# Kernel optimization log

Hardware: AMD Instinct MI355X
Metric: run time of the kernel (lower is better)

Reference implementation:

```python
import jax, jax.numpy as jnp
import numpy as np

N, E, F = 32768, 524288, 16          # nodes, edges, num_filters
S_IN, V_IN = 64, 32                  # input irreps: 64x0e + 32x1o  (dim 64 + 96 = 160)
NRBF = 32                            # radial basis size of f_ij
LN2 = float(np.log(2.0))

def ssp(x):
    # shifted softplus, the standard SchNet activation
    return jax.nn.softplus(x) - LN2

def setup_inputs() -> dict:
    key = jax.random.key(0)
    ks = jax.random.split(key, 16)
    x = jax.random.normal(ks[0], (N, S_IN + 3 * V_IN), jnp.float32)
    idx_i = jax.random.randint(ks[1], (E,), 0, N)
    idx_j = jax.random.randint(ks[2], (E,), 0, N)
    f_ij = jax.random.normal(ks[3], (E, NRBF), jnp.float32)
    rcut_ij = jax.random.uniform(ks[4], (E,), jnp.float32)
    Yr_ij = jax.random.normal(ks[5], (E, 4), jnp.float32)  # 1x0e + 1x1o
    # equivariant Linear 1: (64x0e+32x1o) -> num_filters*(1x0e+1x1o) = 16x0e+16x1o
    W1_0e = jax.random.normal(ks[6], (S_IN, F), jnp.float32)
    W1_1o = jax.random.normal(ks[7], (V_IN, F), jnp.float32)
    # filter MLP: NRBF -> F -> num_irreps(6*F)
    mW1 = jax.random.normal(ks[8], (NRBF, F), jnp.float32) / np.sqrt(NRBF)
    mb1 = jnp.zeros((F,), jnp.float32)
    mW2 = jax.random.normal(ks[9], (F, 6 * F), jnp.float32) / np.sqrt(F)
    mb2 = jnp.zeros((6 * F,), jnp.float32)
    # equivariant Linear 2: (2Fx0e+2Fx1o+Fx1e+Fx2e) -> input irreps (1e/2e paths drop)
    W2_0e = jax.random.normal(ks[10], (2 * F, S_IN), jnp.float32)
    W2_1o = jax.random.normal(ks[11], (2 * F, V_IN), jnp.float32)
    # equivariant Linear 3: input irreps -> input irreps
    W3_0e = jax.random.normal(ks[12], (S_IN, S_IN), jnp.float32)
    W3_1o = jax.random.normal(ks[13], (V_IN, V_IN), jnp.float32)
    return dict(x=x, f_ij=f_ij, rcut_ij=rcut_ij, Yr_ij=Yr_ij,
                W1_0e=W1_0e, W1_1o=W1_1o, mW1=mW1, mb1=mb1, mW2=mW2, mb2=mb2,
                W2_0e=W2_0e, W2_1o=W2_1o, W3_0e=W3_0e, W3_1o=W3_1o,
                idx_i=idx_i, idx_j=idx_j)

def reference(x, f_ij, rcut_ij, Yr_ij, W1_0e, W1_1o, mW1, mb1, mW2, mb2,
              W2_0e, W2_1o, W3_0e, W3_1o, idx_i, idx_j):
    n = x.shape[0]
    s = x[:, :S_IN]                                  # [N, 64]  0e channels
    v = x[:, S_IN:].reshape(n, V_IN, 3)              # [N, 32, 3] 1o channels
    # Linear 1 (per-irrep channel mixing, e3nn fan-in normalization)
    s1 = (s @ W1_0e) / np.sqrt(S_IN)                 # [N, F]
    v1 = jnp.einsum('ncd,cf->nfd', v, W1_1o) / np.sqrt(V_IN)  # [N, F, 3]
    # gather neighbor features (x_j = x[idx_j], mul_to_axis -> per-filter irreps)
    sj = s1[idx_j]                                   # [E, F]
    vj = v1[idx_j]                                   # [E, F, 3]
    y0 = Yr_ij[:, 0]                                 # [E]
    y1 = Yr_ij[:, 1:4]                               # [E, 3]
    # tensor product (0e+1o) x (0e+1o) -> 2x0e + 2x1o + 1x1e + 1x2e, per filter
    o0a = sj * y0[:, None]                                            # 0e: 0e x 0e
    o0b = jnp.einsum('efd,ed->ef', vj, y1) / np.sqrt(3.0)             # 0e: 1o.1o
    o1a = sj[:, :, None] * y1[:, None, :]                             # 1o: 0e x 1o
    o1b = vj * y0[:, None, None]                                      # 1o: 1o x 0e
    o1e = jnp.cross(vj, y1[:, None, :]) / np.sqrt(2.0)                # 1e: 1o ^ 1o
    ux, uy, uz = vj[..., 0], vj[..., 1], vj[..., 2]
    wx, wy, wz = y1[:, None, 0], y1[:, None, 1], y1[:, None, 2]
    o2 = jnp.stack([(ux * wy + uy * wx) / np.sqrt(2.0),
                    (uy * wz + uz * wy) / np.sqrt(2.0),
                    (2.0 * uz * wz - ux * wx - uy * wy) / np.sqrt(6.0),
                    (ux * wz + uz * wx) / np.sqrt(2.0),
                    (ux * wx - uy * wy) / np.sqrt(2.0)], axis=-1)      # 2e [E, F, 5]
    # filter MLP on radial features, gated by cutoff; one scalar per irrep
    W = ssp(f_ij @ mW1 + mb1) @ mW2 + mb2            # [E, 6F]
    W = W * rcut_ij[:, None]
    w0a, w0b, w1a, w1b, w1e, w2 = (W[:, k * F:(k + 1) * F] for k in range(6))
    seg = lambda z: jax.ops.segment_sum(z, idx_i, num_segments=N)
    # modulate + scatter-sum into center atoms
    n0a = seg(o0a * w0a); n0b = seg(o0b * w0b)                          # [N, F]
    n1a = seg(o1a * w1a[:, :, None]); n1b = seg(o1b * w1b[:, :, None])  # [N, F, 3]
    n1e = seg(o1e * w1e[:, :, None])                                    # [N, F, 3] (dropped by Linear 2)
    n2 = seg(o2 * w2[:, :, None])                                       # [N, F, 5] (dropped by Linear 2)
    n0 = jnp.concatenate([n0a, n0b], axis=-1)        # [N, 2F] 0e
    n1 = jnp.concatenate([n1a, n1b], axis=1)         # [N, 2F, 3] 1o
    del n1e, n2  # no matching output irrep in input_irreps -> e3nn Linear drops them
    # Linear 2 back to input irreps
    s2 = (n0 @ W2_0e) / np.sqrt(2 * F)               # [N, 64]
    v2 = jnp.einsum('nfd,fc->ncd', n1, W2_1o) / np.sqrt(2 * F)  # [N, 32, 3]
    # scalar activation on l=0 only
    s2 = ssp(s2)
    # Linear 3
    s3 = (s2 @ W3_0e) / np.sqrt(S_IN)
    v3 = jnp.einsum('ncd,ce->ned', v2, W3_1o) / np.sqrt(V_IN)
    return jnp.concatenate([s3, v3.reshape(n, -1)], axis=-1)  # [N, 160]
```

## Files before the change

### kernel.cpp

```cpp
#include <hip/hip_runtime.h>
#include <math.h>

#define NN 32768
#define NE 524288
#define RSTR 32
#define SREC_STR 36

__device__ __forceinline__ float sspf(float x) {
    const float INVLN2 = 1.4426950408889634f;
    const float LN2    = 0.69314718055994530942f;
    float t = __builtin_amdgcn_exp2f(-fabsf(x) * INVLN2);
    return fmaxf(x, 0.0f) + LN2 * __builtin_amdgcn_logf(1.0f + t) - LN2;
}

__global__ __launch_bounds__(256) void hist_kernel(
    const int* __restrict__ idx_i, int* __restrict__ counts, int* __restrict__ rank)
{
    int e = blockIdx.x * 256 + threadIdx.x;
    rank[e] = atomicAdd(&counts[idx_i[e]], 1);
}

__global__ __launch_bounds__(1024) void scan_kernel(
    const int* __restrict__ counts, int* __restrict__ start, int* __restrict__ order)
{
    __shared__ int tmp[1024];
    __shared__ int bins[64];
    __shared__ int bcur[64];
    int tid = threadIdx.x;
    int base = tid * 32;
    int cnt[32];
    int local[32];
    int sum = 0;
    const int4* c4 = (const int4*)(counts + base);
#pragma unroll
    for (int q = 0; q < 8; q++) {
        int4 v = c4[q];
        cnt[q*4+0] = v.x; cnt[q*4+1] = v.y; cnt[q*4+2] = v.z; cnt[q*4+3] = v.w;
        local[q*4+0] = sum; sum += v.x;
        local[q*4+1] = sum; sum += v.y;
        local[q*4+2] = sum; sum += v.z;
        local[q*4+3] = sum; sum += v.w;
    }
    tmp[tid] = sum;
    __syncthreads();
    for (int off = 1; off < 1024; off <<= 1) {
        int v = 0;
        if (tid >= off) v = tmp[tid - off];
        __syncthreads();
        if (tid >= off) tmp[tid] += v;
        __syncthreads();
    }
    int excl = tmp[tid] - sum;
#pragma unroll
    for (int k = 0; k < 32; k++) {
        start[base + k] = excl + local[k];
    }
    if (tid == 1023) start[NN] = tmp[1023];

    if (tid < 64) bins[tid] = 0;
    __syncthreads();
#pragma unroll
    for (int k = 0; k < 32; k++) {
        int d = cnt[k] > 63 ? 63 : cnt[k];
        atomicAdd(&bins[63 - d], 1);
    }
    __syncthreads();
    if (tid == 0) {
        int run = 0;
        for (int b = 0; b < 64; b++) { int c = bins[b]; bcur[b] = run; run += c; }
    }
    __syncthreads();
#pragma unroll
    for (int k = 0; k < 32; k++) {
        int d = cnt[k] > 63 ? 63 : cnt[k];
        int pos = atomicAdd(&bcur[63 - d], 1);
        order[pos] = base + k;
    }
}

__global__ __launch_bounds__(256) void pack_kernel(
    const float* __restrict__ f_ij,
    const float* __restrict__ rcut_ij,
    const float* __restrict__ Yr,
    const int*   __restrict__ idx_i,
    const int*   __restrict__ idx_j,
    const float* __restrict__ mW1,
    const float* __restrict__ mb1,
    const int*   __restrict__ start,
    const int*   __restrict__ rank,
    float* __restrict__ epack)
{
    __shared__ float sW1[512];
    __shared__ float sb1[16];
    __shared__ float srec[256 * SREC_STR];
    __shared__ int   sslot[256];
    int t = threadIdx.x;
    for (int k = t; k < 512; k += 256) sW1[k] = mW1[k];
    if (t < 16) sb1[t] = mb1[t];
    __syncthreads();

    int e = blockIdx.x * 256 + t;
    float h[16];
#pragma unroll
    for (int f = 0; f < 16; f++) h[f] = sb1[f];
    const float4* frow = (const float4*)(f_ij + (size_t)e * 32);
#pragma unroll
    for (int rq = 0; rq < 8; rq++) {
        float4 fv = frow[rq];
        int r = rq * 4;
#pragma unroll
        for (int f = 0; f < 16; f++)
            h[f] += fv.x * sW1[(r+0)*16+f] + fv.y * sW1[(r+1)*16+f]
                  + fv.z * sW1[(r+2)*16+f] + fv.w * sW1[(r+3)*16+f];
    }
    float rc = rcut_ij[e];
#pragma unroll
    for (int f = 0; f < 16; f++) h[f] = sspf(h[f]) * rc;

    int i = idx_i[e];
    int j = idx_j[e];
    float4 y = ((const float4*)Yr)[e];
    int slot = start[i] + rank[e];

    float* rp = srec + t * SREC_STR;
    float4* rp4 = (float4*)rp;
#pragma unroll
    for (int q = 0; q < 4; q++) rp4[q] = ((float4*)h)[q];
    rp4[4] = y;
    float4 tail; tail.x = rc; tail.y = __int_as_float(j); tail.z = 0.f; tail.w = 0.f;
    rp4[5] = tail;
    float4 z; z.x = 0.f; z.y = 0.f; z.z = 0.f; z.w = 0.f;
    rp4[6] = z;
    rp4[7] = z;
    sslot[t] = slot;
    __syncthreads();

    int lane = t & 63;
    int wbase = t & 192;
    int qi = lane & 7;
#pragma unroll
    for (int g = 0; g < 8; g++) {
        int r = wbase + g * 8 + (lane >> 3);
        int s = sslot[r];
        float4 v = ((const float4*)(srec + r * SREC_STR))[qi];
        ((float4*)(epack + (size_t)s * RSTR))[qi] = v;
    }
}

__global__ __launch_bounds__(256) void embed_kernel(
    const float* __restrict__ x,
    const float* __restrict__ W1s,
    const float* __restrict__ W1v,
    float* __restrict__ embed)
{
    __shared__ float sWs[1024];
    __shared__ float sWv[512];
    int t = threadIdx.x;
    for (int k = t; k < 1024; k += 256) sWs[k] = W1s[k];
    for (int k = t; k < 512;  k += 256) sWv[k] = W1v[k];
    __syncthreads();

    int n = blockIdx.x * 256 + t;
    const float* xr = x + (size_t)n * 160;

    float s1[16];
#pragma unroll
    for (int f = 0; f < 16; f++) s1[f] = 0.f;
#pragma unroll 1
    for (int cc = 0; cc < 4; cc++) {
        float4 sv[4];
#pragma unroll
        for (int q = 0; q < 4; q++) sv[q] = ((const float4*)xr)[cc*4 + q];
#pragma unroll
        for (int q = 0; q < 4; q++) {
            int c = (cc*4 + q) * 4;
#pragma unroll
            for (int f = 0; f < 16; f++) {
                s1[f] += sv[q].x * sWs[(c+0)*16+f] + sv[q].y * sWs[(c+1)*16+f]
                       + sv[q].z * sWs[(c+2)*16+f] + sv[q].w * sWs[(c+3)*16+f];
            }
        }
    }

    float v1[48];
#pragma unroll
    for (int k = 0; k < 48; k++) v1[k] = 0.f;
#pragma unroll 1
    for (int cc = 0; cc < 4; cc++) {
        float4 vv[6];
#pragma unroll
        for (int q = 0; q < 6; q++) vv[q] = ((const float4*)(xr + 64))[cc*6 + q];
#pragma unroll
        for (int q = 0; q < 6; q++) {
            float vals[4] = {vv[q].x, vv[q].y, vv[q].z, vv[q].w};
#pragma unroll
            for (int u = 0; u < 4; u++) {
                int ml = q * 4 + u;
                int c = cc * 8 + ml / 3;
                int d = ml % 3;
                float val = vals[u];
#pragma unroll
                for (int f = 0; f < 16; f++)
                    v1[f*3+d] += val * sWv[c*16+f];
            }
        }
    }

    float ob[64];
    const float is32 = 0.17677669529663688f;
#pragma unroll
    for (int f = 0; f < 16; f++) {
        ob[f*4+0] = s1[f] * 0.125f;
        ob[f*4+1] = v1[f*3+0] * is32;
        ob[f*4+2] = v1[f*3+1] * is32;
        ob[f*4+3] = v1[f*3+2] * is32;
    }

    float4* eo = (float4*)(embed + (size_t)n * 64);
#pragma unroll
    for (int q = 0; q < 16; q++) eo[q] = ((float4*)ob)[q];
}

__global__ __launch_bounds__(256, 4) void nodeagg_kernel(
    const float* __restrict__ embed,
    const float* __restrict__ epack,
    const int*   __restrict__ start,
    const int*   __restrict__ order,
    const float* __restrict__ mW2,
    const float* __restrict__ mb2,
    float* __restrict__ acc)
{
    int t = threadIdx.x;
    int gid = blockIdx.x * 256 + t;
    int node = order[gid >> 4];
    int f = gid & 15;

    float wga[16], wgb[16], wgc[16], wgd[16];
#pragma unroll
    for (int k = 0; k < 16; k++) {
        wga[k] = mW2[k*96 + f];
        wgb[k] = mW2[k*96 + 16 + f];
        wgc[k] = mW2[k*96 + 32 + f];
        wgd[k] = mW2[k*96 + 48 + f];
    }
    float b0a = mb2[f], b0b = mb2[16+f], b1a = mb2[32+f], b1b = mb2[48+f];

    float aa = 0.f, ab = 0.f;
    float A1a0 = 0.f, A1a1 = 0.f, A1a2 = 0.f;
    float A1b0 = 0.f, A1b1 = 0.f, A1b2 = 0.f;

    int s0 = start[node];
    int s1 = start[node+1];

    for (int q = s0; q < s1; q++) {
        const float4* r4 = (const float4*)(epack + (size_t)q * RSTR);
        float4 h0 = r4[0], h1 = r4[1], h2 = r4[2], h3 = r4[3];
        float4 y  = r4[4], tl = r4[5];
        int j = __float_as_int(tl.y);
        float4 e4 = ((const float4*)(embed + (size_t)j * 64))[f];
        float rc = tl.x;

        float w0a = rc*b0a, w0b = rc*b0b, w1a = rc*b1a, w1b = rc*b1b;
        w0a += h0.x*wga[0]  + h0.y*wga[1]  + h0.z*wga[2]  + h0.w*wga[3]
             + h1.x*wga[4]  + h1.y*wga[5]  + h1.z*wga[6]  + h1.w*wga[7]
             + h2.x*wga[8]  + h2.y*wga[9]  + h2.z*wga[10] + h2.w*wga[11]
             + h3.x*wga[12] + h3.y*wga[13] + h3.z*wga[14] + h3.w*wga[15];
        w0b += h0.x*wgb[0]  + h0.y*wgb[1]  + h0.z*wgb[2]  + h0.w*wgb[3]
             + h1.x*wgb[4]  + h1.y*wgb[5]  + h1.z*wgb[6]  + h1.w*wgb[7]
             + h2.x*wgb[8]  + h2.y*wgb[9]  + h2.z*wgb[10] + h2.w*wgb[11]
             + h3.x*wgb[12] + h3.y*wgb[13] + h3.z*wgb[14] + h3.w*wgb[15];
        w1a += h0.x*wgc[0]  + h0.y*wgc[1]  + h0.z*wgc[2]  + h0.w*wgc[3]
             + h1.x*wgc[4]  + h1.y*wgc[5]  + h1.z*wgc[6]  + h1.w*wgc[7]
             + h2.x*wgc[8]  + h2.y*wgc[9]  + h2.z*wgc[10] + h2.w*wgc[11]
             + h3.x*wgc[12] + h3.y*wgc[13] + h3.z*wgc[14] + h3.w*wgc[15];
        w1b += h0.x*wgd[0]  + h0.y*wgd[1]  + h0.z*wgd[2]  + h0.w*wgd[3]
             + h1.x*wgd[4]  + h1.y*wgd[5]  + h1.z*wgd[6]  + h1.w*wgd[7]
             + h2.x*wgd[8]  + h2.y*wgd[9]  + h2.z*wgd[10] + h2.w*wgd[11]
             + h3.x*wgd[12] + h3.y*wgd[13] + h3.z*wgd[14] + h3.w*wgd[15];

        float sj = e4.x, vx = e4.y, vy = e4.z, vz = e4.w;
        aa += sj * y.x * w0a;
        ab += (vx*y.y + vy*y.z + vz*y.w) * w0b;
        float sw = sj * w1a;
        A1a0 += sw * y.y;
        A1a1 += sw * y.z;
        A1a2 += sw * y.w;
        float yw = y.x * w1b;
        A1b0 += vx * yw;
        A1b1 += vy * yw;
        A1b2 += vz * yw;
    }

    const float is3 = 0.5773502691896258f;
    float* o = acc + (size_t)node * 128;
    o[f]       = aa;
    o[16 + f]  = ab * is3;
    o[32 + f]  = A1a0;
    o[48 + f]  = A1a1;
    o[64 + f]  = A1a2;
    o[80 + f]  = A1b0;
    o[96 + f]  = A1b1;
    o[112 + f] = A1b2;
}


__device__ __forceinline__ void v2_seg32(const float* a, int d, int cb,
    const float* __restrict__ W2v, float* V2, int ln)
{
    cb = __builtin_amdgcn_readfirstlane(cb);
    const float is32 = 0.17677669529663688f;
    float na[16], nb[16];
    const float4* pa = (const float4*)(a + 32 + 16*d);
    const float4* pb = (const float4*)(a + 80 + 16*d);
#pragma unroll
    for (int q = 0; q < 4; q++) { ((float4*)na)[q] = pa[q]; ((float4*)nb)[q] = pb[q]; }
    float tacc[32];
#pragma unroll
    for (int c = 0; c < 32; c++) tacc[c] = 0.f;
#pragma unroll
    for (int f = 0; f < 16; f++) {
        float fa = na[f], fb = nb[f];
#pragma unroll
        for (int c = 0; c < 32; c++)
            tacc[c] += fa * W2v[f*32 + cb + c] + fb * W2v[(16+f)*32 + cb + c];
    }
    float* row = V2 + (d*64 + ln) * 33 + cb;
#pragma unroll
    for (int c = 0; c < 32; c++) row[c] = tacc[c] * is32;
}

__device__ __forceinline__ void v2_seg16(const float* a, int d, int cb,
    const float* __restrict__ W2v, float* V2, int ln)
{
    cb = __builtin_amdgcn_readfirstlane(cb);
    const float is32 = 0.17677669529663688f;
    float na[16], nb[16];
    const float4* pa = (const float4*)(a + 32 + 16*d);
    const float4* pb = (const float4*)(a + 80 + 16*d);
#pragma unroll
    for (int q = 0; q < 4; q++) { ((float4*)na)[q] = pa[q]; ((float4*)nb)[q] = pb[q]; }
    float tacc[16];
#pragma unroll
    for (int c = 0; c < 16; c++) tacc[c] = 0.f;
#pragma unroll
    for (int f = 0; f < 16; f++) {
        float fa = na[f], fb = nb[f];
#pragma unroll
        for (int c = 0; c < 16; c++)
            tacc[c] += fa * W2v[f*32 + cb + c] + fb * W2v[(16+f)*32 + cb + c];
    }
    float* row = V2 + (d*64 + ln) * 33 + cb;
#pragma unroll
    for (int c = 0; c < 16; c++) row[c] = tacc[c] * is32;
}

__device__ __forceinline__ void v3_seg32(float* o, int d, int cb,
    const float* __restrict__ W3v, const float* V2, int ln)
{
    cb = __builtin_amdgcn_readfirstlane(cb);
    const float is32 = 0.17677669529663688f;
    float tacc[32];
#pragma unroll
    for (int c = 0; c < 32; c++) tacc[c] = 0.f;
    const float* row = V2 + (d*64 + ln) * 33;
#pragma unroll
    for (int k = 0; k < 32; k++) {
        float vk = row[k];
#pragma unroll
        for (int c = 0; c < 32; c++) tacc[c] += vk * W3v[k*32 + cb + c];
    }
#pragma unroll
    for (int c = 0; c < 32; c++) o[64 + (cb+c)*3 + d] = tacc[c] * is32;
}

__device__ __forceinline__ void v3_seg16(float* o, int d, int cb,
    const float* __restrict__ W3v, const float* V2, int ln)
{
    cb = __builtin_amdgcn_readfirstlane(cb);
    const float is32 = 0.17677669529663688f;
    float tacc[16];
#pragma unroll
    for (int c = 0; c < 16; c++) tacc[c] = 0.f;
    const float* row = V2 + (d*64 + ln) * 33;
#pragma unroll
    for (int k = 0; k < 32; k++) {
        float vk = row[k];
#pragma unroll
        for (int c = 0; c < 16; c++) tacc[c] += vk * W3v[k*32 + cb + c];
    }
#pragma unroll
    for (int c = 0; c < 16; c++) o[64 + (cb+c)*3 + d] = tacc[c] * is32;
}

__global__ __launch_bounds__(256) void out_kernel(
    const float* __restrict__ acc,
    const float* __restrict__ W2s,
    const float* __restrict__ W2v,
    const float* __restrict__ W3s,
    const float* __restrict__ W3v,
    float* __restrict__ out)
{
    __shared__ float S2[64*65];
    __shared__ float V2[3*64*33];
    int t = threadIdx.x;
    int w = t >> 6, ln = t & 63;
    int node = blockIdx.x * 64 + ln;
    const float* a = acc + (size_t)node * 128;
    float* o = out + (size_t)node * 160;
    const float is32 = 0.17677669529663688f;

    if (w < 2) {
        int cb = __builtin_amdgcn_readfirstlane(w * 32);
        float n0r[32];
#pragma unroll
        for (int q = 0; q < 8; q++) ((float4*)n0r)[q] = ((const float4*)a)[q];
        float tacc[32];
#pragma unroll
        for (int c = 0; c < 32; c++) tacc[c] = 0.f;
#pragma unroll
        for (int k = 0; k < 32; k++) {
            float nk = n0r[k];
#pragma unroll
            for (int c = 0; c < 32; c++) tacc[c] += nk * W2s[k*64 + cb + c];
        }
        float* row = S2 + ln*65 + cb;
#pragma unroll
        for (int c = 0; c < 32; c++) row[c] = sspf(tacc[c] * is32);
    } else if (w == 2) {
        v2_seg32(a, 0, 0,  W2v, V2, ln);
        v2_seg16(a, 1, 0,  W2v, V2, ln);
    } else {
        v2_seg16(a, 1, 16, W2v, V2, ln);
        v2_seg32(a, 2, 0,  W2v, V2, ln);
    }
    __syncthreads();
    if (w < 2) {
        int cb = __builtin_amdgcn_readfirstlane(w * 32);
        float tacc[32];
#pragma unroll
        for (int c = 0; c < 32; c++) tacc[c] = 0.f;
        const float* row = S2 + ln*65;
#pragma unroll
        for (int k = 0; k < 64; k++) {
            float sk = row[k];
#pragma unroll
            for (int c = 0; c < 32; c++) tacc[c] += sk * W3s[k*64 + cb + c];
        }
#pragma unroll
        for (int q = 0; q < 8; q++) {
            float4 r = {tacc[q*4+0]*0.125f, tacc[q*4+1]*0.125f,
                        tacc[q*4+2]*0.125f, tacc[q*4+3]*0.125f};
            ((float4*)(o + cb))[q] = r;
        }
    } else if (w == 2) {
        v3_seg32(o, 0, 0,  W3v, V2, ln);
        v3_seg16(o, 1, 0,  W3v, V2, ln);
    } else {
        v3_seg16(o, 1, 16, W3v, V2, ln);
        v3_seg32(o, 2, 0,  W3v, V2, ln);
    }
}

extern "C" void kernel_launch(void* const* d_in, const int* in_sizes, int n_in,
                              void* d_out, int out_size, void* d_ws, size_t ws_size,
                              hipStream_t stream) {
    const float* x     = (const float*)d_in[0];
    const float* f_ij  = (const float*)d_in[1];
    const float* rcut  = (const float*)d_in[2];
    const float* Yr    = (const float*)d_in[3];
    const float* W1s   = (const float*)d_in[4];
    const float* W1v   = (const float*)d_in[5];
    const float* mW1   = (const float*)d_in[6];
    const float* mb1   = (const float*)d_in[7];
    const float* mW2   = (const float*)d_in[8];
    const float* mb2   = (const float*)d_in[9];
    const float* W2s   = (const float*)d_in[10];
    const float* W2v   = (const float*)d_in[11];
    const float* W3s   = (const float*)d_in[12];
    const float* W3v   = (const float*)d_in[13];
    const int*   idx_i = (const int*)d_in[14];
    const int*   idx_j = (const int*)d_in[15];
    float* out = (float*)d_out;

    float* fws   = (float*)d_ws;
    float* embed = fws;
    float* acc   = embed + (size_t)NN * 64;
    float* epack = acc   + (size_t)NN * 128;
    int* ibase   = (int*)(epack + (size_t)NE * RSTR);
    int* counts  = ibase;
    int* start   = counts + NN;
    int* rank    = start + NN + 1;
    int* order   = rank + NE;

    hipMemsetAsync(counts, 0, (size_t)NN * sizeof(int), stream);
    hist_kernel<<<NE/256, 256, 0, stream>>>(idx_i, counts, rank);
    scan_kernel<<<1, 1024, 0, stream>>>(counts, start, order);
    pack_kernel<<<NE/256, 256, 0, stream>>>(f_ij, rcut, Yr, idx_i, idx_j,
                                            mW1, mb1, start, rank, epack);
    embed_kernel<<<NN/256, 256, 0, stream>>>(x, W1s, W1v, embed);
    nodeagg_kernel<<<(NN*16)/256, 256, 0, stream>>>(embed, epack, start, order,
                                                    mW2, mb2, acc);
    out_kernel<<<NN/64, 256, 0, stream>>>(acc, W2s, W2v, W3s, W3v, out);
}
```

Baseline: 333.7 us.

## Halve pack staging LDS and split out_kernel work across eight waves

The pack kernel now stages edge records through a 128-row shared buffer in two passes, each followed by a barrier. This halves LDS use per block so more blocks can be resident. The out kernel moves to 512 threads with eight waves, so each wave keeps smaller accumulator arrays (16 or 24 columns instead of 32). That should lower register pressure and raise occupancy, at the cost of extra barriers and more duplicated reads of the acc rows.

```diff
diff --git a/kernel.cpp b/kernel.cpp
--- a/kernel.cpp
+++ b/kernel.cpp
@@ -92,8 +92,8 @@
 {
     __shared__ float sW1[512];
     __shared__ float sb1[16];
-    __shared__ float srec[256 * SREC_STR];
-    __shared__ int   sslot[256];
+    __shared__ float srec[128 * SREC_STR];
+    __shared__ int   sslot[128];
     int t = threadIdx.x;
     for (int k = t; k < 512; k += 256) sW1[k] = mW1[k];
     if (t < 16) sb1[t] = mb1[t];
@@ -122,28 +122,34 @@
     float4 y = ((const float4*)Yr)[e];
     int slot = start[i] + rank[e];
 
-    float* rp = srec + t * SREC_STR;
-    float4* rp4 = (float4*)rp;
-#pragma unroll
-    for (int q = 0; q < 4; q++) rp4[q] = ((float4*)h)[q];
-    rp4[4] = y;
-    float4 tail; tail.x = rc; tail.y = __int_as_float(j); tail.z = 0.f; tail.w = 0.f;
-    rp4[5] = tail;
-    float4 z; z.x = 0.f; z.y = 0.f; z.z = 0.f; z.w = 0.f;
-    rp4[6] = z;
-    rp4[7] = z;
-    sslot[t] = slot;
-    __syncthreads();
-
-    int lane = t & 63;
-    int wbase = t & 192;
-    int qi = lane & 7;
-#pragma unroll
-    for (int g = 0; g < 8; g++) {
-        int r = wbase + g * 8 + (lane >> 3);
-        int s = sslot[r];
-        float4 v = ((const float4*)(srec + r * SREC_STR))[qi];
-        ((float4*)(epack + (size_t)s * RSTR))[qi] = v;
+#pragma unroll 1
+    for (int p = 0; p < 2; p++) {
+        if ((t >> 7) == p) {
+            int r = t & 127;
+            float* rp = srec + r * SREC_STR;
+            float4* rp4 = (float4*)rp;
+#pragma unroll
+            for (int q = 0; q < 4; q++) rp4[q] = ((float4*)h)[q];
+            rp4[4] = y;
+            float4 tail; tail.x = rc; tail.y = __int_as_float(j);
+            tail.z = 0.f; tail.w = 0.f;
+            rp4[5] = tail;
+            float4 z; z.x = 0.f; z.y = 0.f; z.z = 0.f; z.w = 0.f;
+            rp4[6] = z;
+            rp4[7] = z;
+            sslot[r] = slot;
+        }
+        __syncthreads();
+#pragma unroll
+        for (int g = 0; g < 4; g++) {
+            int idx = g * 256 + t;
+            int r = idx >> 3;
+            int qi = idx & 7;
+            int s = sslot[r];
+            float4 v = ((const float4*)(srec + r * SREC_STR))[qi];
+            ((float4*)(epack + (size_t)s * RSTR))[qi] = v;
+        }
+        __syncthreads();
     }
 }
 
@@ -304,95 +310,55 @@
 }
 
 
-__device__ __forceinline__ void v2_seg32(const float* a, int d, int cb,
+template<int LEN>
+__device__ __forceinline__ void v2_seg(const float* a, int d, int cb,
     const float* __restrict__ W2v, float* V2, int ln)
 {
     cb = __builtin_amdgcn_readfirstlane(cb);
+    d  = __builtin_amdgcn_readfirstlane(d);
     const float is32 = 0.17677669529663688f;
     float na[16], nb[16];
     const float4* pa = (const float4*)(a + 32 + 16*d);
     const float4* pb = (const float4*)(a + 80 + 16*d);
 #pragma unroll
     for (int q = 0; q < 4; q++) { ((float4*)na)[q] = pa[q]; ((float4*)nb)[q] = pb[q]; }
-    float tacc[32];
-#pragma unroll
-    for (int c = 0; c < 32; c++) tacc[c] = 0.f;
+    float tacc[LEN];
+#pragma unroll
+    for (int c = 0; c < LEN; c++) tacc[c] = 0.f;
 #pragma unroll
     for (int f = 0; f < 16; f++) {
         float fa = na[f], fb = nb[f];
 #pragma unroll
-        for (int c = 0; c < 32; c++)
+        for (int c = 0; c < LEN; c++)
             tacc[c] += fa * W2v[f*32 + cb + c] + fb * W2v[(16+f)*32 + cb + c];
     }
     float* row = V2 + (d*64 + ln) * 33 + cb;
 #pragma unroll
-    for (int c = 0; c < 32; c++) row[c] = tacc[c] * is32;
-}
-
-__device__ __forceinline__ void v2_seg16(const float* a, int d, int cb,
-    const float* __restrict__ W2v, float* V2, int ln)
+    for (int c = 0; c < LEN; c++) row[c] = tacc[c] * is32;
+}
+
+template<int LEN>
+__device__ __forceinline__ void v3_seg(float* o, int d, int cb,
+    const float* __restrict__ W3v, const float* V2, int ln)
 {
     cb = __builtin_amdgcn_readfirstlane(cb);
+    d  = __builtin_amdgcn_readfirstlane(d);
     const float is32 = 0.17677669529663688f;
-    float na[16], nb[16];
-    const float4* pa = (const float4*)(a + 32 + 16*d);
-    const float4* pb = (const float4*)(a + 80 + 16*d);
-#pragma unroll
-    for (int q = 0; q < 4; q++) { ((float4*)na)[q] = pa[q]; ((float4*)nb)[q] = pb[q]; }
-    float tacc[16];
-#pragma unroll
-    for (int c = 0; c < 16; c++) tacc[c] = 0.f;
-#pragma unroll
-    for (int f = 0; f < 16; f++) {
-        float fa = na[f], fb = nb[f];
-#pragma unroll
-        for (int c = 0; c < 16; c++)
-            tacc[c] += fa * W2v[f*32 + cb + c] + fb * W2v[(16+f)*32 + cb + c];
-    }
-    float* row = V2 + (d*64 + ln) * 33 + cb;
-#pragma unroll
-    for (int c = 0; c < 16; c++) row[c] = tacc[c] * is32;
-}
-
-__device__ __forceinline__ void v3_seg32(float* o, int d, int cb,
-    const float* __restrict__ W3v, const float* V2, int ln)
-{
-    cb = __builtin_amdgcn_readfirstlane(cb);
-    const float is32 = 0.17677669529663688f;
-    float tacc[32];
-#pragma unroll
-    for (int c = 0; c < 32; c++) tacc[c] = 0.f;
+    float tacc[LEN];
+#pragma unroll
+    for (int c = 0; c < LEN; c++) tacc[c] = 0.f;
     const float* row = V2 + (d*64 + ln) * 33;
 #pragma unroll
     for (int k = 0; k < 32; k++) {
         float vk = row[k];
 #pragma unroll
-        for (int c = 0; c < 32; c++) tacc[c] += vk * W3v[k*32 + cb + c];
-    }
-#pragma unroll
-    for (int c = 0; c < 32; c++) o[64 + (cb+c)*3 + d] = tacc[c] * is32;
-}
-
-__device__ __forceinline__ void v3_seg16(float* o, int d, int cb,
-    const float* __restrict__ W3v, const float* V2, int ln)
-{
-    cb = __builtin_amdgcn_readfirstlane(cb);
-    const float is32 = 0.17677669529663688f;
-    float tacc[16];
-#pragma unroll
-    for (int c = 0; c < 16; c++) tacc[c] = 0.f;
-    const float* row = V2 + (d*64 + ln) * 33;
-#pragma unroll
-    for (int k = 0; k < 32; k++) {
-        float vk = row[k];
-#pragma unroll
-        for (int c = 0; c < 16; c++) tacc[c] += vk * W3v[k*32 + cb + c];
-    }
-#pragma unroll
-    for (int c = 0; c < 16; c++) o[64 + (cb+c)*3 + d] = tacc[c] * is32;
-}
-
-__global__ __launch_bounds__(256) void out_kernel(
+        for (int c = 0; c < LEN; c++) tacc[c] += vk * W3v[k*32 + cb + c];
+    }
+#pragma unroll
+    for (int c = 0; c < LEN; c++) o[64 + (cb+c)*3 + d] = tacc[c] * is32;
+}
+
+__global__ __launch_bounds__(512, 4) void out_kernel(
     const float* __restrict__ acc,
     const float* __restrict__ W2s,
     const float* __restrict__ W2v,
@@ -409,55 +375,63 @@
     float* o = out + (size_t)node * 160;
     const float is32 = 0.17677669529663688f;
 
-    if (w < 2) {
-        int cb = __builtin_amdgcn_readfirstlane(w * 32);
+    if (w < 4) {
+        int cb = __builtin_amdgcn_readfirstlane(w * 16);
         float n0r[32];
 #pragma unroll
         for (int q = 0; q < 8; q++) ((float4*)n0r)[q] = ((const float4*)a)[q];
-        float tacc[32];
-#pragma unroll
-        for (int c = 0; c < 32; c++) tacc[c] = 0.f;
+        float tacc[16];
+#pragma unroll
+        for (int c = 0; c < 16; c++) tacc[c] = 0.f;
 #pragma unroll
         for (int k = 0; k < 32; k++) {
             float nk = n0r[k];
 #pragma unroll
-            for (int c = 0; c < 32; c++) tacc[c] += nk * W2s[k*64 + cb + c];
+            for (int c = 0; c < 16; c++) tacc[c] += nk * W2s[k*64 + cb + c];
         }
         float* row = S2 + ln*65 + cb;
 #pragma unroll
-        for (int c = 0; c < 32; c++) row[c] = sspf(tacc[c] * is32);
-    } else if (w == 2) {
-        v2_seg32(a, 0, 0,  W2v, V2, ln);
-        v2_seg16(a, 1, 0,  W2v, V2, ln);
+        for (int c = 0; c < 16; c++) row[c] = sspf(tacc[c] * is32);
+    } else if (w == 4) {
+        v2_seg<24>(a, 0, 0,  W2v, V2, ln);
+    } else if (w == 5) {
+        v2_seg<8> (a, 0, 24, W2v, V2, ln);
+        v2_seg<16>(a, 1, 0,  W2v, V2, ln);
+    } else if (w == 6) {
+        v2_seg<16>(a, 1, 16, W2v, V2, ln);
+        v2_seg<8> (a, 2, 0,  W2v, V2, ln);
     } else {
-        v2_seg16(a, 1, 16, W2v, V2, ln);
-        v2_seg32(a, 2, 0,  W2v, V2, ln);
-    }
-    __syncthreads();
-    if (w < 2) {
-        int cb = __builtin_amdgcn_readfirstlane(w * 32);
-        float tacc[32];
-#pragma unroll
-        for (int c = 0; c < 32; c++) tacc[c] = 0.f;
+        v2_seg<24>(a, 2, 8,  W2v, V2, ln);
+    }
+    __syncthreads();
+    if (w < 4) {
+        int cb = __builtin_amdgcn_readfirstlane(w * 16);
+        float tacc[16];
+#pragma unroll
+        for (int c = 0; c < 16; c++) tacc[c] = 0.f;
         const float* row = S2 + ln*65;
 #pragma unroll
         for (int k = 0; k < 64; k++) {
             float sk = row[k];
 #pragma unroll
-            for (int c = 0; c < 32; c++) tacc[c] += sk * W3s[k*64 + cb + c];
-        }
-#pragma unroll
-        for (int q = 0; q < 8; q++) {
+            for (int c = 0; c < 16; c++) tacc[c] += sk * W3s[k*64 + cb + c];
+        }
+#pragma unroll
+        for (int q = 0; q < 4; q++) {
             float4 r = {tacc[q*4+0]*0.125f, tacc[q*4+1]*0.125f,
                         tacc[q*4+2]*0.125f, tacc[q*4+3]*0.125f};
             ((float4*)(o + cb))[q] = r;
         }
-    } else if (w == 2) {
-        v3_seg32(o, 0, 0,  W3v, V2, ln);
-        v3_seg16(o, 1, 0,  W3v, V2, ln);
+    } else if (w == 4) {
+        v3_seg<24>(o, 0, 0,  W3v, V2, ln);
+    } else if (w == 5) {
+        v3_seg<8> (o, 0, 24, W3v, V2, ln);
+        v3_seg<16>(o, 1, 0,  W3v, V2, ln);
+    } else if (w == 6) {
+        v3_seg<16>(o, 1, 16, W3v, V2, ln);
+        v3_seg<8> (o, 2, 0,  W3v, V2, ln);
     } else {
-        v3_seg16(o, 1, 16, W3v, V2, ln);
-        v3_seg32(o, 2, 0,  W3v, V2, ln);
+        v3_seg<24>(o, 2, 8,  W3v, V2, ln);
     }
 }
 
@@ -500,5 +474,5 @@
     embed_kernel<<<NN/256, 256, 0, stream>>>(x, W1s, W1v, embed);
     nodeagg_kernel<<<(NN*16)/256, 256, 0, stream>>>(embed, epack, start, order,
                                                     mW2, mb2, acc);
-    out_kernel<<<NN/64, 256, 0, stream>>>(acc, W2s, W2v, W3s, W3v, out);
-}
+    out_kernel<<<NN/64, 512, 0, stream>>>(acc, W2s, W2v, W3s, W3v, out);
+}
```

After: 320.7 us. -3.9%, faster.
